# Optimization experiments

Measured on AMD Instinct MI355X. Metric: run time of the kernel, lower is better.

Reference implementation:

```python
import jax, jax.numpy as jnp
import numpy as np

B, IDF, RES = 32, 64, 128
CDF, SRC_L, A_DIM = 768, 18, 100
QUERY_L = RES * RES


def setup_inputs() -> dict:
    key = jax.random.key(0)
    ks = jax.random.split(key, 5)
    inputs = jax.random.normal(ks[0], (B, IDF, RES, RES), dtype=jnp.float32)
    context = jax.random.normal(ks[1], (B, CDF, SRC_L), dtype=jnp.float32)
    conv_ctx_w = jax.random.normal(ks[2], (IDF, CDF), dtype=jnp.float32) * (1.0 / np.sqrt(CDF))
    conv_w = jax.random.normal(ks[3], (IDF,), dtype=jnp.float32) * (1.0 / np.sqrt(IDF))
    conv_b = jnp.zeros((1,), dtype=jnp.float32)
    fc_w = jax.random.normal(ks[4], (A_DIM, QUERY_L), dtype=jnp.float32) * (1.0 / np.sqrt(QUERY_L))
    fc_b = jnp.zeros((A_DIM,), dtype=jnp.float32)
    return {"inputs": inputs, "context": context, "conv_ctx_w": conv_ctx_w,
            "conv_w": conv_w, "conv_b": conv_b, "fc_w": fc_w, "fc_b": fc_b}


def reference(inputs, context, conv_ctx_w, conv_w, conv_b, fc_w, fc_b):
    b, idf, ih, iw = inputs.shape
    queryL = ih * iw
    # target: [b, idf, queryL]
    target = inputs.reshape(b, idf, queryL)
    # 1x1 conv on context (conv_context): [b, idf, sourceL]
    sourceT = jnp.einsum('ic,bcs->bis', conv_ctx_w, context)
    # attn scores: [b, queryL, sourceL]; softmax over sourceL (dim=1 on flattened view)
    attn = jnp.einsum('biq,bis->bqs', target, sourceT)
    attn = jax.nn.softmax(attn, axis=-1)
    # weighted context: [b, idf, queryL]
    wctx = jnp.einsum('bis,bqs->biq', sourceT, attn)
    # 1x1 conv to single channel (self.conv): [b, queryL]
    wctx = jnp.einsum('i,biq->bq', conv_w, wctx) + conv_b
    # att_fc: [b, a_dim]
    out = wctx @ fc_w.T + fc_b
    return out
```

## Files before the change

kernel.cpp:

```cpp
#include <hip/hip_runtime.h>

#define BB 32
#define IDF 64
#define QL 16384
#define CDF 768
#define SL 18
#define SLP 20
#define CLP 21
#define ADIM 100

typedef __attribute__((address_space(3))) unsigned int lds_u32_t;
typedef __attribute__((address_space(1))) const unsigned int glb_u32_t;

__global__ __launch_bounds__(256, 2) void kA_source(
        const float* __restrict__ ctx,
        const float* __restrict__ wic,
        const float* __restrict__ fc_b,
        float* __restrict__ sT,
        float* __restrict__ out)
{
    __shared__ float ctx_l[CDF * CLP];
    const int blk  = blockIdx.x;
    const int tid  = threadIdx.x;
    const int wave = tid >> 6;
    const int lane = tid & 63;
    const int b = blk >> 4;
    const int g = blk & 15;

    if (blk < 13) {
        const int t = blk * 256 + tid;
        if (t < BB * ADIM) out[t] = fc_b[t % ADIM];
    }

    const float* ctxb = ctx + (size_t)b * CDF * SL;
    for (int t = tid; t < CDF * SL; t += 256) {
        const int c = t / SL;
        const int s = t - c * SL;
        ctx_l[c * CLP + s] = ctxb[t];
    }
    __syncthreads();

    const int i = g * 4 + wave;
    const float* wrow = wic + (size_t)i * CDF;

    float acc[SL];
#pragma unroll
    for (int s = 0; s < SL; s++) acc[s] = 0.f;

#pragma unroll 2
    for (int k = 0; k < CDF / 64; k++) {
        const int c = k * 64 + lane;
        const float wv = wrow[c];
#pragma unroll
        for (int s = 0; s < SL; s++) acc[s] += wv * ctx_l[c * CLP + s];
    }
#pragma unroll
    for (int s = 0; s < SL; s++) {
        float a = acc[s];
#pragma unroll
        for (int off = 32; off; off >>= 1) a += __shfl_xor(a, off, 64);
        if (lane == 0) sT[((size_t)b * IDF + i) * SLP + s] = a;
    }
}

__global__ __launch_bounds__(256, 4) void kB_attn(
        const float* __restrict__ inp,
        const float* __restrict__ sT,
        const float* __restrict__ conv_w,
        const float* __restrict__ conv_b,
        const float* __restrict__ fcw,
        float* __restrict__ out)
{
    __shared__ __align__(16) float xbuf[2][8][512];
    __shared__ float v_l[SL];
    __shared__ __align__(16) float wq_l[512];
    const int b   = blockIdx.y;
    const int qt  = blockIdx.x;
    const int tid = threadIdx.x;
    const int wave = tid >> 6;
    const int lane = tid & 63;
    const float* st = sT + (size_t)b * IDF * SLP;

    if (tid < SL) {
        float a = 0.f;
        for (int i = 0; i < IDF; i++) a += conv_w[i] * st[i * SLP + tid];
        v_l[tid] = a;
    }

    const float* gbase = inp + (size_t)b * IDF * QL + (size_t)qt * 512;

#define STAGE(st_idx, buf)                                                              \
    {                                                                                   \
        const int i0_ = (st_idx) * 8;                                                   \
        _Pragma("unroll")                                                               \
        for (int c_ = 0; c_ < 4; c_++) {                                                \
            const int j_ = wave * 4 + c_;                                               \
            const int r_ = j_ >> 1, h_ = j_ & 1;                                        \
            const float* g_ = gbase + (size_t)(i0_ + r_) * QL + h_ * 256 + lane * 4;    \
            float* l_ = &xbuf[(buf)][r_][h_ * 256];                                     \
            __builtin_amdgcn_global_load_lds((glb_u32_t*)g_, (lds_u32_t*)l_, 16, 0, 0); \
        }                                                                               \
    }

    STAGE(0, 0);

    float2 sc[SL];
#pragma unroll
    for (int s = 0; s < SL; s++) sc[s] = make_float2(0.f, 0.f);

#pragma unroll 1
    for (int k = 0; k < 8; k++) {
        __syncthreads();
        if (k < 7) STAGE(k + 1, (k + 1) & 1);
        const int kb = k & 1;
#pragma unroll
        for (int r = 0; r < 8; r++) {
            const int i = k * 8 + r;
            const float x0 = xbuf[kb][r][tid];
            const float x1 = xbuf[kb][r][tid + 256];
            const float* strow = st + i * SLP;
#pragma unroll
            for (int s = 0; s < SL; s++) {
                const float rs = strow[s];
                sc[s].x += x0 * rs;
                sc[s].y += x1 * rs;
            }
        }
    }

    float2 m = sc[0];
#pragma unroll
    for (int s = 1; s < SL; s++) {
        m.x = fmaxf(m.x, sc[s].x);
        m.y = fmaxf(m.y, sc[s].y);
    }
    float2 l = make_float2(0.f, 0.f);
    float2 o = make_float2(0.f, 0.f);
#pragma unroll
    for (int s = 0; s < SL; s++) {
        const float vs = v_l[s];
        float2 p;
        p.x = __expf(sc[s].x - m.x);
        p.y = __expf(sc[s].y - m.y);
        l.x += p.x; l.y += p.y;
        o.x += p.x * vs; o.y += p.y * vs;
    }
    const float cb = conv_b[0];
    wq_l[tid]       = o.x / l.x + cb;
    wq_l[tid + 256] = o.y / l.y + cb;
    __syncthreads();

    const float4 w0 = *(const float4*)(&wq_l[lane * 4]);
    const float4 w1 = *(const float4*)(&wq_l[256 + lane * 4]);
    const float* fbase = fcw + (size_t)qt * 512 + lane * 4;
#pragma unroll 2
    for (int j = 0; j < 25; j++) {
        const int a = j * 4 + wave;
        const float4 f0 = *(const float4*)(fbase + (size_t)a * QL);
        const float4 f1 = *(const float4*)(fbase + (size_t)a * QL + 256);
        float r = f0.x * w0.x + f0.y * w0.y + f0.z * w0.z + f0.w * w0.w
                + f1.x * w1.x + f1.y * w1.y + f1.z * w1.z + f1.w * w1.w;
#pragma unroll
        for (int off = 32; off; off >>= 1) r += __shfl_xor(r, off, 64);
        if (lane == 0) atomicAdd(&out[b * ADIM + a], r);
    }
}

extern "C" void kernel_launch(void* const* d_in, const int* in_sizes, int n_in,
                              void* d_out, int out_size, void* d_ws, size_t ws_size,
                              hipStream_t stream)
{
    const float* inputs     = (const float*)d_in[0];
    const float* context    = (const float*)d_in[1];
    const float* conv_ctx_w = (const float*)d_in[2];
    const float* conv_w     = (const float*)d_in[3];
    const float* conv_b     = (const float*)d_in[4];
    const float* fc_w       = (const float*)d_in[5];
    const float* fc_b       = (const float*)d_in[6];
    float* out = (float*)d_out;

    float* ws = (float*)d_ws;
    float* sT = ws;

    kA_source<<<dim3(512), dim3(256), 0, stream>>>(context, conv_ctx_w, fc_b, sT, out);
    kB_attn<<<dim3(32, BB), dim3(256), 0, stream>>>(inputs, sT, conv_w, conv_b, fc_w, out);
}
```

Before: 239.7 us.

## Replace LDS-staged input tiles with register double-buffered direct global loads

Drops the async global-to-LDS staging and its per-stage barriers in the attention kernel. Each thread now loads adjacent query pairs as float2 straight into registers, ping-ponging two 8-row register buffers so loads overlap with the score FMAs. Each thread now owns queries 2*tid and 2*tid+1, so the wq_l write indexing changes to match. This removes LDS traffic and barriers but raises register pressure and makes each load instruction narrower.

```diff
diff --git a/kernel.cpp b/kernel.cpp
--- a/kernel.cpp
+++ b/kernel.cpp
@@ -8,9 +8,6 @@
 #define SLP 20
 #define CLP 21
 #define ADIM 100
-
-typedef __attribute__((address_space(3))) unsigned int lds_u32_t;
-typedef __attribute__((address_space(1))) const unsigned int glb_u32_t;
 
 __global__ __launch_bounds__(256, 2) void kA_source(
         const float* __restrict__ ctx,
@@ -71,7 +68,6 @@
         const float* __restrict__ fcw,
         float* __restrict__ out)
 {
-    __shared__ __align__(16) float xbuf[2][8][512];
     __shared__ float v_l[SL];
     __shared__ __align__(16) float wq_l[512];
     const int b   = blockIdx.y;
@@ -87,46 +83,45 @@
         v_l[tid] = a;
     }
 
-    const float* gbase = inp + (size_t)b * IDF * QL + (size_t)qt * 512;
-
-#define STAGE(st_idx, buf)                                                              \
-    {                                                                                   \
-        const int i0_ = (st_idx) * 8;                                                   \
-        _Pragma("unroll")                                                               \
-        for (int c_ = 0; c_ < 4; c_++) {                                                \
-            const int j_ = wave * 4 + c_;                                               \
-            const int r_ = j_ >> 1, h_ = j_ & 1;                                        \
-            const float* g_ = gbase + (size_t)(i0_ + r_) * QL + h_ * 256 + lane * 4;    \
-            float* l_ = &xbuf[(buf)][r_][h_ * 256];                                     \
-            __builtin_amdgcn_global_load_lds((glb_u32_t*)g_, (lds_u32_t*)l_, 16, 0, 0); \
-        }                                                                               \
-    }
-
-    STAGE(0, 0);
+    const float* gq = inp + (size_t)b * IDF * QL + (size_t)qt * 512 + 2 * tid;
 
     float2 sc[SL];
 #pragma unroll
     for (int s = 0; s < SL; s++) sc[s] = make_float2(0.f, 0.f);
 
-#pragma unroll 1
-    for (int k = 0; k < 8; k++) {
-        __syncthreads();
-        if (k < 7) STAGE(k + 1, (k + 1) & 1);
-        const int kb = k & 1;
-#pragma unroll
-        for (int r = 0; r < 8; r++) {
-            const int i = k * 8 + r;
-            const float x0 = xbuf[kb][r][tid];
-            const float x1 = xbuf[kb][r][tid + 256];
-            const float* strow = st + i * SLP;
-#pragma unroll
-            for (int s = 0; s < SL; s++) {
-                const float rs = strow[s];
-                sc[s].x += x0 * rs;
-                sc[s].y += x1 * rs;
-            }
-        }
+    float2 xa[8], xb[8];
+
+#define LOADG(dst, base_i)                                                   \
+    _Pragma("unroll")                                                        \
+    for (int r_ = 0; r_ < 8; r_++)                                           \
+        dst[r_] = *(const float2*)(gq + (size_t)((base_i) + r_) * QL);
+
+#define FMAG(src, base_i)                                                    \
+    _Pragma("unroll")                                                        \
+    for (int r_ = 0; r_ < 8; r_++) {                                         \
+        const float* strow_ = st + ((base_i) + r_) * SLP;       \
+        _Pragma("unroll")                                                    \
+        for (int s_ = 0; s_ < SL; s_++) {                                    \
+            const float rs_ = strow_[s_];                                    \
+            sc[s_].x += src[r_].x * rs_;                                     \
+            sc[s_].y += src[r_].y * rs_;                                     \
+        }                                                                    \
     }
+
+    LOADG(xa, 0)
+    LOADG(xb, 8)
+    FMAG(xa, 0)  LOADG(xa, 16)
+    FMAG(xb, 8)  LOADG(xb, 24)
+    FMAG(xa, 16) LOADG(xa, 32)
+    FMAG(xb, 24) LOADG(xb, 40)
+    FMAG(xa, 32) LOADG(xa, 48)
+    FMAG(xb, 40) LOADG(xb, 56)
+    FMAG(xa, 48)
+    FMAG(xb, 56)
+#undef LOADG
+#undef FMAG
+
+    __syncthreads();
 
     float2 m = sc[0];
 #pragma unroll
@@ -146,8 +141,8 @@
         o.x += p.x * vs; o.y += p.y * vs;
     }
     const float cb = conv_b[0];
-    wq_l[tid]       = o.x / l.x + cb;
-    wq_l[tid + 256] = o.y / l.y + cb;
+    wq_l[2 * tid]     = o.x / l.x + cb;
+    wq_l[2 * tid + 1] = o.y / l.y + cb;
     __syncthreads();
 
     const float4 w0 = *(const float4*)(&wq_l[lane * 4]);
```

After: 244.2 us. About the same (+1.9%).

## Load inputs directly to registers with prefetch, stage sT in LDS, 512 threads

Applied to the files above, without the earlier changes.

The attention kernel no longer stages input tiles through LDS with async global_load_lds and per-chunk barriers. Each thread now owns a single query and prefetches the next 8 channels into registers while computing on the current 8. The per-batch source matrix is copied into LDS once and read as float4 broadcasts instead of from global memory. The block grows to 512 threads with a higher occupancy hint, which trades register-level double buffering for possible register pressure and spills.

```diff
diff --git a/kernel.cpp b/kernel.cpp
--- a/kernel.cpp
+++ b/kernel.cpp
@@ -8,9 +8,6 @@
 #define SLP 20
 #define CLP 21
 #define ADIM 100
-
-typedef __attribute__((address_space(3))) unsigned int lds_u32_t;
-typedef __attribute__((address_space(1))) const unsigned int glb_u32_t;
 
 __global__ __launch_bounds__(256, 2) void kA_source(
         const float* __restrict__ ctx,
@@ -63,7 +60,7 @@
     }
 }
 
-__global__ __launch_bounds__(256, 4) void kB_attn(
+__global__ __launch_bounds__(512, 8) void kB_attn(
         const float* __restrict__ inp,
         const float* __restrict__ sT,
         const float* __restrict__ conv_w,
@@ -71,7 +68,7 @@
         const float* __restrict__ fcw,
         float* __restrict__ out)
 {
-    __shared__ __align__(16) float xbuf[2][8][512];
+    __shared__ __align__(16) float st_l[IDF * SLP];
     __shared__ float v_l[SL];
     __shared__ __align__(16) float wq_l[512];
     const int b   = blockIdx.y;
@@ -79,90 +76,89 @@
     const int tid = threadIdx.x;
     const int wave = tid >> 6;
     const int lane = tid & 63;
-    const float* st = sT + (size_t)b * IDF * SLP;
+
+    {
+        const float* stg = sT + (size_t)b * IDF * SLP;
+#pragma unroll
+        for (int t = tid; t < IDF * SLP; t += 512) st_l[t] = stg[t];
+    }
+    __syncthreads();
 
     if (tid < SL) {
         float a = 0.f;
-        for (int i = 0; i < IDF; i++) a += conv_w[i] * st[i * SLP + tid];
+        for (int i = 0; i < IDF; i++) a += conv_w[i] * st_l[i * SLP + tid];
         v_l[tid] = a;
     }
 
-    const float* gbase = inp + (size_t)b * IDF * QL + (size_t)qt * 512;
+    const float* gq = inp + (size_t)b * IDF * QL + (size_t)qt * 512 + tid;
 
-#define STAGE(st_idx, buf)                                                              \
-    {                                                                                   \
-        const int i0_ = (st_idx) * 8;                                                   \
-        _Pragma("unroll")                                                               \
-        for (int c_ = 0; c_ < 4; c_++) {                                                \
-            const int j_ = wave * 4 + c_;                                               \
-            const int r_ = j_ >> 1, h_ = j_ & 1;                                        \
-            const float* g_ = gbase + (size_t)(i0_ + r_) * QL + h_ * 256 + lane * 4;    \
-            float* l_ = &xbuf[(buf)][r_][h_ * 256];                                     \
-            __builtin_amdgcn_global_load_lds((glb_u32_t*)g_, (lds_u32_t*)l_, 16, 0, 0); \
-        }                                                                               \
+    float sc[SL];
+#pragma unroll
+    for (int s = 0; s < SL; s++) sc[s] = 0.f;
+
+    float xcur[8], xnxt[8];
+#pragma unroll
+    for (int r = 0; r < 8; r++) xcur[r] = gq[(size_t)r * QL];
+
+#pragma unroll
+    for (int k = 0; k < 8; k++) {
+        if (k < 7) {
+#pragma unroll
+            for (int r = 0; r < 8; r++) xnxt[r] = gq[(size_t)(k * 8 + 8 + r) * QL];
+        }
+#pragma unroll
+        for (int r = 0; r < 8; r++) {
+            const float* row_ = &st_l[(k * 8 + r) * SLP];
+            const float4 t0 = *(const float4*)(row_ + 0);
+            const float4 t1 = *(const float4*)(row_ + 4);
+            const float4 t2 = *(const float4*)(row_ + 8);
+            const float4 t3 = *(const float4*)(row_ + 12);
+            const float2 t4 = *(const float2*)(row_ + 16);
+            const float xv = xcur[r];
+            sc[0]  += xv * t0.x;  sc[1]  += xv * t0.y;
+            sc[2]  += xv * t0.z;  sc[3]  += xv * t0.w;
+            sc[4]  += xv * t1.x;  sc[5]  += xv * t1.y;
+            sc[6]  += xv * t1.z;  sc[7]  += xv * t1.w;
+            sc[8]  += xv * t2.x;  sc[9]  += xv * t2.y;
+            sc[10] += xv * t2.z;  sc[11] += xv * t2.w;
+            sc[12] += xv * t3.x;  sc[13] += xv * t3.y;
+            sc[14] += xv * t3.z;  sc[15] += xv * t3.w;
+            sc[16] += xv * t4.x;  sc[17] += xv * t4.y;
+        }
+#pragma unroll
+        for (int r = 0; r < 8; r++) xcur[r] = xnxt[r];
     }
 
-    STAGE(0, 0);
+    __syncthreads();
 
-    float2 sc[SL];
+    float m = sc[0];
 #pragma unroll
-    for (int s = 0; s < SL; s++) sc[s] = make_float2(0.f, 0.f);
-
-#pragma unroll 1
-    for (int k = 0; k < 8; k++) {
-        __syncthreads();
-        if (k < 7) STAGE(k + 1, (k + 1) & 1);
-        const int kb = k & 1;
-#pragma unroll
-        for (int r = 0; r < 8; r++) {
-            const int i = k * 8 + r;
-            const float x0 = xbuf[kb][r][tid];
-            const float x1 = xbuf[kb][r][tid + 256];
-            const float* strow = st + i * SLP;
-#pragma unroll
-            for (int s = 0; s < SL; s++) {
-                const float rs = strow[s];
-                sc[s].x += x0 * rs;
-                sc[s].y += x1 * rs;
-            }
-        }
-    }
-
-    float2 m = sc[0];
-#pragma unroll
-    for (int s = 1; s < SL; s++) {
-        m.x = fmaxf(m.x, sc[s].x);
-        m.y = fmaxf(m.y, sc[s].y);
-    }
-    float2 l = make_float2(0.f, 0.f);
-    float2 o = make_float2(0.f, 0.f);
+    for (int s = 1; s < SL; s++) m = fmaxf(m, sc[s]);
+    float l = 0.f, o = 0.f;
 #pragma unroll
     for (int s = 0; s < SL; s++) {
-        const float vs = v_l[s];
-        float2 p;
-        p.x = __expf(sc[s].x - m.x);
-        p.y = __expf(sc[s].y - m.y);
-        l.x += p.x; l.y += p.y;
-        o.x += p.x * vs; o.y += p.y * vs;
+        const float p = __expf(sc[s] - m);
+        l += p;
+        o += p * v_l[s];
     }
-    const float cb = conv_b[0];
-    wq_l[tid]       = o.x / l.x + cb;
-    wq_l[tid + 256] = o.y / l.y + cb;
+    wq_l[tid] = o / l + conv_b[0];
     __syncthreads();
 
     const float4 w0 = *(const float4*)(&wq_l[lane * 4]);
     const float4 w1 = *(const float4*)(&wq_l[256 + lane * 4]);
     const float* fbase = fcw + (size_t)qt * 512 + lane * 4;
 #pragma unroll 2
-    for (int j = 0; j < 25; j++) {
-        const int a = j * 4 + wave;
-        const float4 f0 = *(const float4*)(fbase + (size_t)a * QL);
-        const float4 f1 = *(const float4*)(fbase + (size_t)a * QL + 256);
-        float r = f0.x * w0.x + f0.y * w0.y + f0.z * w0.z + f0.w * w0.w
-                + f1.x * w1.x + f1.y * w1.y + f1.z * w1.z + f1.w * w1.w;
+    for (int j = 0; j < 13; j++) {
+        const int a = j * 8 + wave;
+        if (a < ADIM) {
+            const float4 f0 = *(const float4*)(fbase + (size_t)a * QL);
+            const float4 f1 = *(const float4*)(fbase + (size_t)a * QL + 256);
+            float r = f0.x * w0.x + f0.y * w0.y + f0.z * w0.z + f0.w * w0.w
+                    + f1.x * w1.x + f1.y * w1.y + f1.z * w1.z + f1.w * w1.w;
 #pragma unroll
-        for (int off = 32; off; off >>= 1) r += __shfl_xor(r, off, 64);
-        if (lane == 0) atomicAdd(&out[b * ADIM + a], r);
+            for (int off = 32; off; off >>= 1) r += __shfl_xor(r, off, 64);
+            if (lane == 0) atomicAdd(&out[b * ADIM + a], r);
+        }
     }
 }
 
@@ -183,5 +179,5 @@
     float* sT = ws;
 
     kA_source<<<dim3(512), dim3(256), 0, stream>>>(context, conv_ctx_w, fc_b, sT, out);
-    kB_attn<<<dim3(32, BB), dim3(256), 0, stream>>>(inputs, sT, conv_w, conv_b, fc_w, out);
+    kB_attn<<<dim3(32, BB), dim3(512), 0, stream>>>(inputs, sT, conv_w, conv_b, fc_w, out);
 }
```

After: 394.0 us. 1.64x slower.
